# Kernel optimization log

Measured on AMD Instinct MI355X. Metric: run time of the kernel, lower is better.

Reference implementation:

```python
import jax, jax.numpy as jnp
import numpy as np

NEG_SLOPE = 0.01  # F.leaky_relu default


def grid_sample_bilinear(im, pts):
    """torch.nn.functional.grid_sample equivalent, mode='bilinear',
    align_corners=True, padding_mode='zeros'.
    im: [B, C, H, W], pts: [B, N, 2] in [-1, 1] (x, y order). Returns [B, C, N].
    """
    B, C, H, W = im.shape
    x = (pts[..., 0] + 1.0) * 0.5 * (W - 1)  # [B, N]
    y = (pts[..., 1] + 1.0) * 0.5 * (H - 1)
    x0 = jnp.floor(x)
    y0 = jnp.floor(y)
    wx1 = x - x0
    wy1 = y - y0
    wx0 = 1.0 - wx1
    wy0 = 1.0 - wy1
    x0i = x0.astype(jnp.int32)
    y0i = y0.astype(jnp.int32)
    x1i = x0i + 1
    y1i = y0i + 1

    def corner(yi, xi, w):
        valid = (xi >= 0) & (xi < W) & (yi >= 0) & (yi < H)
        yc = jnp.clip(yi, 0, H - 1)
        xc = jnp.clip(xi, 0, W - 1)
        # gather per-batch: [B, C, N]
        g = jax.vmap(lambda f, yy, xx: f[:, yy, xx])(im, yc, xc)
        return g * (w * valid.astype(im.dtype))[:, None, :]

    return (corner(y0i, x0i, wy0 * wx0) + corner(y0i, x1i, wy0 * wx1)
            + corner(y1i, x0i, wy1 * wx0) + corner(y1i, x1i, wy1 * wx1))


def conv1x1(x, w, b):
    # x: [B, Cin, N], w: [Cout, Cin], b: [Cout] -> [B, Cout, N]
    return jnp.einsum('oi,bin->bon', w, x) + b[None, :, None]


def setup_inputs() -> dict:
    key = jax.random.key(0)
    ks = jax.random.split(key, 9)
    B, N, C, H, W = 64, 6890, 256, 56, 56
    filter_channels = [256, 128, 64, 5]
    points = jax.random.uniform(ks[0], (B, N, 2), jnp.float32, -1.0, 1.0)
    im_feat = jax.random.normal(ks[1], (B, C, H, W), jnp.float32)

    def mk_conv(k, cin, cout):
        k1, k2 = jax.random.split(k)
        bound = 1.0 / np.sqrt(cin)
        w = jax.random.uniform(k1, (cout, cin), jnp.float32, -bound, bound)
        b = jax.random.uniform(k2, (cout,), jnp.float32, -bound, bound)
        return w, b

    w0, b0 = mk_conv(ks[2], filter_channels[0], filter_channels[1])
    w1, b1 = mk_conv(ks[3], filter_channels[1] + filter_channels[0], filter_channels[2])
    w2, b2 = mk_conv(ks[4], filter_channels[2] + filter_channels[0], filter_channels[3])
    return {"points": points, "im_feat": im_feat,
            "w0": w0, "b0": b0, "w1": w1, "b1": b1, "w2": w2, "b2": b2}


def reference(points, im_feat, w0, b0, w1, b1, w2, b2):
    # sampling: bilinear gather of point-wise features, [B, C_s, N]
    point_feat = grid_sample_bilinear(im_feat, points)
    # reduce_dim: 1x1 conv MLP with skip-concat of the input features
    y = jax.nn.leaky_relu(conv1x1(point_feat, w0, b0), NEG_SLOPE)
    y = jax.nn.leaky_relu(conv1x1(jnp.concatenate([y, point_feat], axis=1), w1, b1), NEG_SLOPE)
    y = conv1x1(jnp.concatenate([y, point_feat], axis=1), w2, b2)  # last layer: no leaky_relu
    y = jax.nn.relu(y)  # self.last_op
    mesh_align_feat = y.reshape(y.shape[0], -1)  # [B, C_p * N]
    return (mesh_align_feat, point_feat)
```

## Files before the change

kernel.cpp:

```cpp
#include <hip/hip_runtime.h>

#define B_    64
#define C_    256
#define H_    56
#define W_    56
#define N_    6890
#define HW_   3136
#define NTILE 108

#define WB1_OFF (128*256)
#define WB2_OFF (128*256 + 64*384)
#define WTOT    (128*256 + 64*384 + 5*320)

typedef __attribute__((ext_vector_type(8))) __bf16 bf16x8;
typedef __attribute__((ext_vector_type(8))) unsigned short ushort8;
typedef __attribute__((ext_vector_type(4))) float f32x4;
typedef __attribute__((ext_vector_type(2))) float f32x2;
typedef __attribute__((ext_vector_type(4))) unsigned int uint4v;
typedef __attribute__((ext_vector_type(2))) unsigned int uint2v;

__device__ __forceinline__ unsigned short f2bf(float f) {
    unsigned int u = __builtin_bit_cast(unsigned int, f);
    u += 0x7FFFu + ((u >> 16) & 1u);
    return (unsigned short)(u >> 16);
}
__device__ __forceinline__ unsigned int pack2(float lo, float hi) {
    return (unsigned int)f2bf(lo) | ((unsigned int)f2bf(hi) << 16);
}
__device__ __forceinline__ float leaky(float v) { return v > 0.f ? v : 0.01f * v; }
__device__ __forceinline__ int pswz(int p) { return p ^ ((p >> 3) & 7); }

__global__ void wconv_kernel(const float* __restrict__ w0, const float* __restrict__ w1,
                             const float* __restrict__ w2, unsigned short* __restrict__ wb) {
    int i = blockIdx.x * 256 + threadIdx.x;
    if (i >= WTOT) return;
    float v = (i < WB1_OFF) ? w0[i] : (i < WB2_OFF) ? w1[i - WB1_OFF] : w2[i - WB2_OFF];
    wb[i] = f2bf(v);
}

__global__ __launch_bounds__(256) void transpose_kernel(
    const float* __restrict__ im, float* __restrict__ imT) {
    __shared__ float Lt[64][68];
    const int t   = threadIdx.x;
    const int bid = blockIdx.x;
    const int xcd  = bid & 7;
    const int rest = bid >> 3;
    const int b    = ((rest & 7) << 3) + xcd;
    const int tl   = rest >> 3;
    const int pt   = tl % 49, ct = tl / 49;
    const int p0   = pt * 64, c0 = ct * 64;

    const float* src = im + ((size_t)b * C_ + c0) * HW_ + p0;
#pragma unroll
    for (int rr = 0; rr < 4; rr++) {
        int c_loc = (t >> 4) + rr * 16;
        int pq    = (t & 15) << 2;
        f32x4 v = *(const f32x4*)(src + (size_t)c_loc * HW_ + pq);
        Lt[c_loc][pq]     = v[0];
        Lt[c_loc][pq + 1] = v[1];
        Lt[c_loc][pq + 2] = v[2];
        Lt[c_loc][pq + 3] = v[3];
    }
    __syncthreads();
    float* dst = imT + ((size_t)b * HW_ + p0) * C_ + c0;
#pragma unroll
    for (int i = 0; i < 4; i++) {
        int idx = t + (i << 8);
        int pr  = idx >> 4;
        int c4  = (idx & 15) << 2;
        f32x4 v;
        v[0] = Lt[c4][pr]; v[1] = Lt[c4 + 1][pr];
        v[2] = Lt[c4 + 2][pr]; v[3] = Lt[c4 + 3][pr];
        *(f32x4*)(dst + (size_t)pr * C_ + c4) = v;
    }
}

__device__ __forceinline__ bf16x8 bfrag(const unsigned int* buf, int rowstride_dw,
                                        int n, int k0) {
    int cd = (k0 >> 1) ^ ((n & 7) << 2);
    uint4v v = *(const uint4v*)(buf + n * rowstride_dw + cd);
    return __builtin_bit_cast(bf16x8, v);
}
__device__ __forceinline__ bf16x8 afrag_bf(const unsigned short* __restrict__ wb, int ldk,
                                           int rowbase, int k0, int lane, int nrows) {
    int i = rowbase + (lane & 15);
    int k = k0 + ((lane >> 4) << 3);
    if (i < nrows) return __builtin_bit_cast(bf16x8, *(const ushort8*)(wb + (size_t)i * ldk + k));
    ushort8 z = {0, 0, 0, 0, 0, 0, 0, 0};
    return __builtin_bit_cast(bf16x8, z);
}

__global__ __launch_bounds__(256, 2) void fused_kernel(
    const float* __restrict__ points, const float* __restrict__ imT,
    const float* __restrict__ b0_, const float* __restrict__ b1,
    const float* __restrict__ b2, const unsigned short* __restrict__ wb,
    float* __restrict__ out0, float* __restrict__ out1) {
    __shared__ float Ls[16384];
    __shared__ float Pw[64][4];
    __shared__ int   Pi[64][2];

    const int t    = threadIdx.x;
    const int lane = t & 63;
    const int wave = t >> 6;
    const int bid  = blockIdx.x;
    const int xcd  = bid & 7;
    const int rr   = bid >> 3;
    const int tile = rr % NTILE;
    const int b    = (rr / NTILE) * 8 + xcd;
    const int n0   = tile * 64;

    if (t < 64) {
        int n = min(n0 + t, N_ - 1);
        f32x2 pt = *(const f32x2*)(points + ((size_t)b * N_ + n) * 2);
        float fx = fminf(fmaxf((pt.x + 1.f) * 27.5f, 0.f), 55.f);
        float fy = fminf(fmaxf((pt.y + 1.f) * 27.5f, 0.f), 55.f);
        float x0f = floorf(fx), y0f = floorf(fy);
        int x0 = (int)x0f, y0 = (int)y0f;
        float wx1 = fx - x0f, wy1 = fy - y0f;
        float wx0 = 1.f - wx1, wy0 = 1.f - wy1;
        bool hix = x0 >= W_ - 1;
        int   xb  = hix ? W_ - 2 : x0;
        float wxl = hix ? 0.f : wx0;
        float wxr = hix ? wx0 : wx1;
        int y0c = min(y0, H_ - 1);
        int y1c = min(y0 + 1, H_ - 1);
        Pw[t][0] = wy0 * wxl; Pw[t][1] = wy0 * wxr;
        Pw[t][2] = wy1 * wxl; Pw[t][3] = wy1 * wxr;
        Pi[t][0] = y0c * W_ + xb; Pi[t][1] = y1c * W_ + xb;
    }
    __syncthreads();

    const float* ib = imT + (size_t)b * HW_ * C_;
#pragma unroll
    for (int i = 0; i < 16; i += 2) {
        int pA = wave * 16 + i, pB = pA + 1;
        float wA0 = Pw[pA][0], wA1 = Pw[pA][1], wA2 = Pw[pA][2], wA3 = Pw[pA][3];
        float wB0 = Pw[pB][0], wB1 = Pw[pB][1], wB2 = Pw[pB][2], wB3 = Pw[pB][3];
        int aA0 = Pi[pA][0], aA1 = Pi[pA][1];
        int aB0 = Pi[pB][0], aB1 = Pi[pB][1];
        const float* sA0 = ib + ((size_t)aA0 << 8) + (lane << 2);
        const float* sA1 = ib + ((size_t)aA1 << 8) + (lane << 2);
        const float* sB0 = ib + ((size_t)aB0 << 8) + (lane << 2);
        const float* sB1 = ib + ((size_t)aB1 << 8) + (lane << 2);
        f32x4 cA00 = *(const f32x4*)(sA0);
        f32x4 cA01 = *(const f32x4*)(sA0 + 256);
        f32x4 cA10 = *(const f32x4*)(sA1);
        f32x4 cA11 = *(const f32x4*)(sA1 + 256);
        f32x4 cB00 = *(const f32x4*)(sB0);
        f32x4 cB01 = *(const f32x4*)(sB0 + 256);
        f32x4 cB10 = *(const f32x4*)(sB1);
        f32x4 cB11 = *(const f32x4*)(sB1 + 256);
        f32x4 vA, vB;
#pragma unroll
        for (int j = 0; j < 4; j++) {
            vA[j] = wA0 * cA00[j] + wA1 * cA01[j] + wA2 * cA10[j] + wA3 * cA11[j];
            vB[j] = wB0 * cB00[j] + wB1 * cB01[j] + wB2 * cB10[j] + wB3 * cB11[j];
        }
        *(f32x4*)(Ls + pA * 256 + ((lane ^ (pA & 7)) << 2)) = vA;
        *(f32x4*)(Ls + pB * 256 + ((lane ^ (pB & 7)) << 2)) = vB;
    }
    __syncthreads();

    f32x4 xr[16];
#pragma unroll
    for (int q = 0; q < 16; q++) {
        int qd = (wave * 16 + q) ^ (lane & 7);
        xr[q] = *(const f32x4*)(Ls + lane * 256 + (qd << 2));
    }
    __syncthreads();

    unsigned int* Xs  = (unsigned int*)Ls;
    unsigned int* Y0s = (unsigned int*)Ls + 8192;
    {
        float* pfb = out1 + (size_t)b * C_ * N_ + n0;
        const bool okn = (n0 + lane) < N_;
        const int swz = (lane & 7) << 2;
#pragma unroll
        for (int q = 0; q < 16; q += 2) {
            int c0 = wave * 64 + q * 4;
            if (okn) {
#pragma unroll
                for (int jj = 0; jj < 4; jj++) {
                    pfb[(size_t)(c0 + jj) * N_ + lane]     = xr[q][jj];
                    pfb[(size_t)(c0 + 4 + jj) * N_ + lane] = xr[q + 1][jj];
                }
            }
            uint4v pk;
            pk[0] = pack2(xr[q][0], xr[q][1]);     pk[1] = pack2(xr[q][2], xr[q][3]);
            pk[2] = pack2(xr[q + 1][0], xr[q + 1][1]); pk[3] = pack2(xr[q + 1][2], xr[q + 1][3]);
            *(uint4v*)(Xs + lane * 128 + ((c0 >> 1) ^ swz)) = pk;
        }
    }

    bf16x8 a1[2][8];
#pragma unroll
    for (int mt = 0; mt < 2; mt++)
#pragma unroll
        for (int ks = 0; ks < 8; ks++)
            a1[mt][ks] = afrag_bf(wb, 256, (wave * 2 + mt) * 16, ks * 32, lane, 1 << 30);

    __syncthreads();

    const int cl = lane & 15;
    const int rh = lane >> 4;
    const int kq = rh << 3;

    f32x4 acc1[2][4] = {};
#pragma unroll
    for (int ks = 0; ks < 8; ks++) {
        bf16x8 bx[4];
#pragma unroll
        for (int nt = 0; nt < 4; nt++)
            bx[nt] = bfrag(Xs, 128, nt * 16 + cl, ks * 32 + kq);
#pragma unroll
        for (int mt = 0; mt < 2; mt++)
#pragma unroll
            for (int nt = 0; nt < 4; nt++)
                acc1[mt][nt] = __builtin_amdgcn_mfma_f32_16x16x32_bf16(
                    a1[mt][ks], bx[nt], acc1[mt][nt], 0, 0, 0);
    }

#pragma unroll
    for (int mt = 0; mt < 2; mt++) {
        int m0 = (wave * 2 + mt) * 16 + (rh << 2);
        f32x4 bias = *(const f32x4*)(b0_ + m0);
#pragma unroll
        for (int nt = 0; nt < 4; nt++) {
            int nn = nt * 16 + cl;
            float v0 = leaky(acc1[mt][nt][0] + bias[0]);
            float v1 = leaky(acc1[mt][nt][1] + bias[1]);
            float v2 = leaky(acc1[mt][nt][2] + bias[2]);
            float v3 = leaky(acc1[mt][nt][3] + bias[3]);
            int md = (m0 >> 1) ^ ((nn & 7) << 2);
            uint2v pk; pk[0] = pack2(v0, v1); pk[1] = pack2(v2, v3);
            *(uint2v*)(Y0s + nn * 64 + md) = pk;
        }
    }

    bf16x8 a2[12];
#pragma unroll
    for (int ks = 0; ks < 12; ks++)
        a2[ks] = afrag_bf(wb + WB1_OFF, 384, wave * 16, ks * 32, lane, 1 << 30);

    __syncthreads();

    f32x4 acc2[4] = {};
#pragma unroll
    for (int ks = 0; ks < 12; ks++) {
#pragma unroll
        for (int nt = 0; nt < 4; nt++) {
            bf16x8 bx = (ks < 4) ? bfrag(Y0s, 64, nt * 16 + cl, ks * 32 + kq)
                                 : bfrag(Xs, 128, nt * 16 + cl, (ks - 4) * 32 + kq);
            acc2[nt] = __builtin_amdgcn_mfma_f32_16x16x32_bf16(a2[ks], bx, acc2[nt], 0, 0, 0);
        }
    }

    bf16x8 a3[10];
#pragma unroll
    for (int ks = 0; ks < 10; ks++)
        a3[ks] = afrag_bf(wb + WB2_OFF, 320, 0, ks * 32, lane, 5);

    __syncthreads();

    {
        int m0 = wave * 16 + (rh << 2);
        f32x4 bias = *(const f32x4*)(b1 + m0);
#pragma unroll
        for (int nt = 0; nt < 4; nt++) {
            int nn = nt * 16 + cl;
            float v0 = leaky(acc2[nt][0] + bias[0]);
            float v1 = leaky(acc2[nt][1] + bias[1]);
            float v2 = leaky(acc2[nt][2] + bias[2]);
            float v3 = leaky(acc2[nt][3] + bias[3]);
            int md = (m0 >> 1) ^ ((nn & 7) << 2);
            uint2v pk; pk[0] = pack2(v0, v1); pk[1] = pack2(v2, v3);
            *(uint2v*)(Y0s + nn * 32 + md) = pk;
        }
    }

    __syncthreads();

    {
        int nn = wave * 16 + cl;
        f32x4 acc3 = {};
#pragma unroll
        for (int ks = 0; ks < 10; ks++) {
            bf16x8 bx = (ks < 2) ? bfrag(Y0s, 32, nn, ks * 32 + kq)
                                 : bfrag(Xs, 128, nn, (ks - 2) * 32 + kq);
            acc3 = __builtin_amdgcn_mfma_f32_16x16x32_bf16(a3[ks], bx, acc3, 0, 0, 0);
        }
        int gn2 = n0 + nn;
        if (gn2 < N_) {
#pragma unroll
            for (int r2 = 0; r2 < 4; r2++) {
                int m = (rh << 2) + r2;
                if (m < 5) {
                    float v = acc3[r2] + b2[m];
                    v = v > 0.f ? v : 0.f;
                    out0[((size_t)b * 5 + m) * N_ + gn2] = v;
                }
            }
        }
    }
}

__global__ __launch_bounds__(512, 6) void gather_kernel(
    const float* __restrict__ points, const float* __restrict__ im,
    float* __restrict__ out1) {
    __shared__ float Lg[HW_ * 4];
    const int t   = threadIdx.x;
    const int bid = blockIdx.x;
    const int b  = ((bid & 7) << 3) | ((bid >> 3) & 7);
    const int ch = bid >> 6;
    const f32x4* im4 = (const f32x4*)(im + ((size_t)b * C_ + ch * 4) * HW_);
#pragma unroll
    for (int g0 = 0; g0 < 2; g0++) {
        int g = t + (g0 << 9);
        if (g < 784) {
            f32x4 r0 = im4[g], r1 = im4[784 + g], r2 = im4[1568 + g], r3 = im4[2352 + g];
#pragma unroll
            for (int i = 0; i < 4; i++) {
                f32x4 v; v[0] = r0[i]; v[1] = r1[i]; v[2] = r2[i]; v[3] = r3[i];
                *(f32x4*)(Lg + (pswz((g << 2) + i) << 2)) = v;
            }
        }
    }
    __syncthreads();
    const float* ptb = points + (size_t)b * N_ * 2;
    const size_t ob0 = ((size_t)b * C_ + ch * 4) * N_;
#pragma unroll 2
    for (int p = 0; p < 14; p++) {
        int n = t + (p << 9);
        if (n < N_) {
            f32x2 pt = *(const f32x2*)(ptb + 2 * n);
            float fx = fminf(fmaxf((pt.x + 1.f) * 27.5f, 0.f), 55.f);
            float fy = fminf(fmaxf((pt.y + 1.f) * 27.5f, 0.f), 55.f);
            float x0f = floorf(fx), y0f = floorf(fy);
            int x0 = (int)x0f, y0 = (int)y0f;
            float wx1 = fx - x0f, wy1 = fy - y0f;
            float wx0 = 1.f - wx1, wy0 = 1.f - wy1;
            bool hix = x0 >= W_ - 1;
            int   xb  = hix ? W_ - 2 : x0;
            float wxl = hix ? 0.f : wx0;
            float wxr = hix ? wx0 : wx1;
            int y0c = min(y0, H_ - 1);
            int y1c = min(y0 + 1, H_ - 1);
            float w00 = wy0 * wxl, w01 = wy0 * wxr, w10 = wy1 * wxl, w11 = wy1 * wxr;
            int ia0 = y0c * W_ + xb, ia1 = y1c * W_ + xb;
            f32x4 q00 = *(const f32x4*)(Lg + (pswz(ia0)     << 2));
            f32x4 q01 = *(const f32x4*)(Lg + (pswz(ia0 + 1) << 2));
            f32x4 q10 = *(const f32x4*)(Lg + (pswz(ia1)     << 2));
            f32x4 q11 = *(const f32x4*)(Lg + (pswz(ia1 + 1) << 2));
            out1[ob0 + n]        = w00*q00[0] + w01*q01[0] + w10*q10[0] + w11*q11[0];
            out1[ob0 + N_ + n]   = w00*q00[1] + w01*q01[1] + w10*q10[1] + w11*q11[1];
            out1[ob0 + 2*N_ + n] = w00*q00[2] + w01*q01[2] + w10*q10[2] + w11*q11[2];
            out1[ob0 + 3*N_ + n] = w00*q00[3] + w01*q01[3] + w10*q10[3] + w11*q11[3];
        }
    }
}

__device__ __forceinline__ bf16x8 afrag_f32(const float* __restrict__ wp, int ldk,
                                            int rowbase, int k0, int lane, int nrows) {
    int i = rowbase + (lane & 15);
    int k = k0 + ((lane >> 4) << 3);
    ushort8 u;
    if (i < nrows) {
        const float* s = wp + (size_t)i * ldk + k;
#pragma unroll
        for (int j = 0; j < 8; j++) u[j] = f2bf(s[j]);
    } else {
#pragma unroll
        for (int j = 0; j < 8; j++) u[j] = 0;
    }
    return __builtin_bit_cast(bf16x8, u);
}

template <bool BF16W>
__global__ __launch_bounds__(256) void mlp_kernel(
    const float* __restrict__ pf,
    const float* __restrict__ w0, const float* __restrict__ b0_,
    const float* __restrict__ w1, const float* __restrict__ b1,
    const float* __restrict__ w2, const float* __restrict__ b2,
    const unsigned short* __restrict__ wb,
    float* __restrict__ out0) {
    __shared__ unsigned int Xs[64 * 128];
    __shared__ unsigned int Y0s[64 * 64];
    const int t    = threadIdx.x;
    const int lane = t & 63;
    const int wave = t >> 6;
    const int bid  = blockIdx.x;
    const int b    = bid / NTILE;
    const int tile = bid - b * NTILE;
    const int n0   = tile * 64;
    const int nn_g = min(n0 + lane, N_ - 1);
    const int swz  = (lane & 7) << 2;
    const float* pfb = pf + (size_t)b * C_ * N_;
#pragma unroll
    for (int g8 = 0; g8 < 8; g8++) {
        int c0 = wave * 64 + g8 * 8;
        float v[8];
#pragma unroll
        for (int j = 0; j < 8; j++) v[j] = pfb[(size_t)(c0 + j) * N_ + nn_g];
        uint4v pk;
        pk[0] = pack2(v[0], v[1]); pk[1] = pack2(v[2], v[3]);
        pk[2] = pack2(v[4], v[5]); pk[3] = pack2(v[6], v[7]);
        *(uint4v*)(Xs + lane * 128 + ((c0 >> 1) ^ swz)) = pk;
    }
    bf16x8 a1[2][8];
#pragma unroll
    for (int mt = 0; mt < 2; mt++)
#pragma unroll
        for (int ks = 0; ks < 8; ks++)
            a1[mt][ks] = BF16W ? afrag_bf(wb, 256, (wave * 2 + mt) * 16, ks * 32, lane, 1 << 30)
                               : afrag_f32(w0, 256, (wave * 2 + mt) * 16, ks * 32, lane, 1 << 30);
    __syncthreads();
    const int cl = lane & 15;
    const int rh = lane >> 4;
    const int kq = rh << 3;
    f32x4 acc1[2][4] = {};
#pragma unroll
    for (int ks = 0; ks < 8; ks++) {
        bf16x8 bx[4];
#pragma unroll
        for (int nt = 0; nt < 4; nt++)
            bx[nt] = bfrag(Xs, 128, nt * 16 + cl, ks * 32 + kq);
#pragma unroll
        for (int mt = 0; mt < 2; mt++)
#pragma unroll
            for (int nt = 0; nt < 4; nt++)
                acc1[mt][nt] = __builtin_amdgcn_mfma_f32_16x16x32_bf16(
                    a1[mt][ks], bx[nt], acc1[mt][nt], 0, 0, 0);
    }
#pragma unroll
    for (int mt = 0; mt < 2; mt++) {
        int m0 = (wave * 2 + mt) * 16 + (rh << 2);
        f32x4 bias = *(const f32x4*)(b0_ + m0);
#pragma unroll
        for (int nt = 0; nt < 4; nt++) {
            int nn = nt * 16 + cl;
            float v0 = leaky(acc1[mt][nt][0] + bias[0]);
            float v1 = leaky(acc1[mt][nt][1] + bias[1]);
            float v2 = leaky(acc1[mt][nt][2] + bias[2]);
            float v3 = leaky(acc1[mt][nt][3] + bias[3]);
            int md = (m0 >> 1) ^ ((nn & 7) << 2);
            uint2v pk; pk[0] = pack2(v0, v1); pk[1] = pack2(v2, v3);
            *(uint2v*)(Y0s + nn * 64 + md) = pk;
        }
    }
    bf16x8 a2[12];
#pragma unroll
    for (int ks = 0; ks < 12; ks++)
        a2[ks] = BF16W ? afrag_bf(wb + WB1_OFF, 384, wave * 16, ks * 32, lane, 1 << 30)
                       : afrag_f32(w1, 384, wave * 16, ks * 32, lane, 1 << 30);
    __syncthreads();
    f32x4 acc2[4] = {};
#pragma unroll
    for (int ks = 0; ks < 12; ks++) {
#pragma unroll
        for (int nt = 0; nt < 4; nt++) {
            bf16x8 bx = (ks < 4) ? bfrag(Y0s, 64, nt * 16 + cl, ks * 32 + kq)
                                 : bfrag(Xs, 128, nt * 16 + cl, (ks - 4) * 32 + kq);
            acc2[nt] = __builtin_amdgcn_mfma_f32_16x16x32_bf16(a2[ks], bx, acc2[nt], 0, 0, 0);
        }
    }
    bf16x8 a3[10];
#pragma unroll
    for (int ks = 0; ks < 10; ks++)
        a3[ks] = BF16W ? afrag_bf(wb + WB2_OFF, 320, 0, ks * 32, lane, 5)
                       : afrag_f32(w2, 320, 0, ks * 32, lane, 5);
    __syncthreads();
    {
        int m0 = wave * 16 + (rh << 2);
        f32x4 bias = *(const f32x4*)(b1 + m0);
#pragma unroll
        for (int nt = 0; nt < 4; nt++) {
            int nn = nt * 16 + cl;
            float v0 = leaky(acc2[nt][0] + bias[0]);
            float v1 = leaky(acc2[nt][1] + bias[1]);
            float v2 = leaky(acc2[nt][2] + bias[2]);
            float v3 = leaky(acc2[nt][3] + bias[3]);
            int md = (m0 >> 1) ^ ((nn & 7) << 2);
            uint2v pk; pk[0] = pack2(v0, v1); pk[1] = pack2(v2, v3);
            *(uint2v*)(Y0s + nn * 32 + md) = pk;
        }
    }
    __syncthreads();
    {
        int nn = wave * 16 + cl;
        f32x4 acc3 = {};
#pragma unroll
        for (int ks = 0; ks < 10; ks++) {
            bf16x8 bx = (ks < 2) ? bfrag(Y0s, 32, nn, ks * 32 + kq)
                                 : bfrag(Xs, 128, nn, (ks - 2) * 32 + kq);
            acc3 = __builtin_amdgcn_mfma_f32_16x16x32_bf16(a3[ks], bx, acc3, 0, 0, 0);
        }
        int gn2 = n0 + nn;
        if (gn2 < N_) {
#pragma unroll
            for (int r2 = 0; r2 < 4; r2++) {
                int m = (rh << 2) + r2;
                if (m < 5) {
                    float v = acc3[r2] + b2[m];
                    v = v > 0.f ? v : 0.f;
                    out0[((size_t)b * 5 + m) * N_ + gn2] = v;
                }
            }
        }
    }
}

extern "C" void kernel_launch(void* const* d_in, const int* in_sizes, int n_in,
                              void* d_out, int out_size, void* d_ws, size_t ws_size,
                              hipStream_t stream) {
    const float* points = (const float*)d_in[0];
    const float* im     = (const float*)d_in[1];
    const float* w0     = (const float*)d_in[2];
    const float* b0     = (const float*)d_in[3];
    const float* w1     = (const float*)d_in[4];
    const float* b1     = (const float*)d_in[5];
    const float* w2     = (const float*)d_in[6];
    const float* b2     = (const float*)d_in[7];
    float* out0 = (float*)d_out;
    float* out1 = out0 + (size_t)B_ * 5 * N_;

    const size_t TBYTES = (size_t)B_ * HW_ * C_ * 4;
    const size_t WBYTES = (size_t)WTOT * 2;
    const bool fok = (d_ws != nullptr) && (ws_size >= TBYTES + WBYTES);
    const bool wok = fok || ((d_ws != nullptr) && (ws_size >= WBYTES));
    float*          imT = (float*)d_ws;
    unsigned short* wb  = fok ? (unsigned short*)((char*)d_ws + TBYTES)
                              : (unsigned short*)d_ws;

    if (wok) {
        hipLaunchKernelGGL(wconv_kernel, dim3((WTOT + 255) / 256), dim3(256), 0, stream,
                           w0, w1, w2, wb);
    }
    if (fok) {
        hipLaunchKernelGGL(transpose_kernel, dim3(B_ * 196), dim3(256), 0, stream, im, imT);
        hipLaunchKernelGGL(fused_kernel, dim3(B_ * NTILE), dim3(256), 0, stream,
                           points, imT, b0, b1, b2, wb, out0, out1);
    } else {
        hipLaunchKernelGGL(gather_kernel, dim3(B_ * 64), dim3(512), 0, stream,
                           points, im, out1);
        if (wok) {
            hipLaunchKernelGGL(mlp_kernel<true>, dim3(B_ * NTILE), dim3(256), 0, stream,
                               out1, w0, b0, w1, b1, w2, b2, wb, out0);
        } else {
            hipLaunchKernelGGL(mlp_kernel<false>, dim3(B_ * NTILE), dim3(256), 0, stream,
                               out1, w0, b0, w1, b1, w2, b2,
                               (const unsigned short*)nullptr, out0);
        }
    }
}
```

Before: 393.0 us.

## Replace image transpose with LDS-staged channel-slice gather into bf16 intermediate

The channel-last fp32 image transpose and the global-memory corner gathers inside the fused kernel are removed. A new gather kernel stages a 4-channel slice of one batch image in LDS, samples every point from LDS, and writes a packed bf16 intermediate. The MLP kernel then reads that intermediate, expands it to fp32 for the point_feat output, and feeds the MFMA layers. This replaces the large transpose round trip and scattered global reads with coalesced streaming. The cost is an extra intermediate write and read, and point_feat values are now rounded to bf16, which reduces output precision.

```diff
diff --git a/kernel.cpp b/kernel.cpp
--- a/kernel.cpp
+++ b/kernel.cpp
@@ -27,6 +27,12 @@
 __device__ __forceinline__ unsigned int pack2(float lo, float hi) {
     return (unsigned int)f2bf(lo) | ((unsigned int)f2bf(hi) << 16);
 }
+__device__ __forceinline__ float bflo(unsigned int u) {
+    return __builtin_bit_cast(float, u << 16);
+}
+__device__ __forceinline__ float bfhi(unsigned int u) {
+    return __builtin_bit_cast(float, u & 0xffff0000u);
+}
 __device__ __forceinline__ float leaky(float v) { return v > 0.f ? v : 0.01f * v; }
 __device__ __forceinline__ int pswz(int p) { return p ^ ((p >> 3) & 7); }
 
@@ -38,49 +44,68 @@
     wb[i] = f2bf(v);
 }
 
-__global__ __launch_bounds__(256) void transpose_kernel(
-    const float* __restrict__ im, float* __restrict__ imT) {
-    __shared__ float Lt[64][68];
+__global__ __launch_bounds__(512, 6) void gather_c(
+    const float* __restrict__ points, const float* __restrict__ im,
+    unsigned int* __restrict__ x2) {
+    __shared__ float Ls[HW_ * 4];
+
     const int t   = threadIdx.x;
     const int bid = blockIdx.x;
-    const int xcd  = bid & 7;
-    const int rest = bid >> 3;
-    const int b    = ((rest & 7) << 3) + xcd;
-    const int tl   = rest >> 3;
-    const int pt   = tl % 49, ct = tl / 49;
-    const int p0   = pt * 64, c0 = ct * 64;
-
-    const float* src = im + ((size_t)b * C_ + c0) * HW_ + p0;
-#pragma unroll
-    for (int rr = 0; rr < 4; rr++) {
-        int c_loc = (t >> 4) + rr * 16;
-        int pq    = (t & 15) << 2;
-        f32x4 v = *(const f32x4*)(src + (size_t)c_loc * HW_ + pq);
-        Lt[c_loc][pq]     = v[0];
-        Lt[c_loc][pq + 1] = v[1];
-        Lt[c_loc][pq + 2] = v[2];
-        Lt[c_loc][pq + 3] = v[3];
-    }
-    __syncthreads();
-    float* dst = imT + ((size_t)b * HW_ + p0) * C_ + c0;
-#pragma unroll
-    for (int i = 0; i < 4; i++) {
-        int idx = t + (i << 8);
-        int pr  = idx >> 4;
-        int c4  = (idx & 15) << 2;
-        f32x4 v;
-        v[0] = Lt[c4][pr]; v[1] = Lt[c4 + 1][pr];
-        v[2] = Lt[c4 + 2][pr]; v[3] = Lt[c4 + 3][pr];
-        *(f32x4*)(dst + (size_t)pr * C_ + c4) = v;
-    }
-}
-
-__device__ __forceinline__ bf16x8 bfrag(const unsigned int* buf, int rowstride_dw,
-                                        int n, int k0) {
-    int cd = (k0 >> 1) ^ ((n & 7) << 2);
-    uint4v v = *(const uint4v*)(buf + n * rowstride_dw + cd);
-    return __builtin_bit_cast(bf16x8, v);
-}
+    const int b  = ((bid & 7) << 3) | ((bid >> 3) & 7);
+    const int ch = bid >> 6;
+
+    const f32x4* im4 = (const f32x4*)(im + ((size_t)b * C_ + ch * 4) * HW_);
+#pragma unroll
+    for (int g0 = 0; g0 < 2; g0++) {
+        int g = t + (g0 << 9);
+        if (g < 784) {
+            f32x4 r0 = im4[g], r1 = im4[784 + g], r2 = im4[1568 + g], r3 = im4[2352 + g];
+#pragma unroll
+            for (int i = 0; i < 4; i++) {
+                f32x4 v; v[0] = r0[i]; v[1] = r1[i]; v[2] = r2[i]; v[3] = r3[i];
+                *(f32x4*)(Ls + (pswz((g << 2) + i) << 2)) = v;
+            }
+        }
+    }
+    __syncthreads();
+
+    const float* ptb = points + (size_t)b * N_ * 2;
+    unsigned int* xout = x2 + ((size_t)((b << 6) + ch) * N_) * 2;
+#pragma unroll 2
+    for (int p = 0; p < 14; p++) {
+        int n = t + (p << 9);
+        if (n < N_) {
+            f32x2 pt = *(const f32x2*)(ptb + 2 * n);
+            float fx = fminf(fmaxf((pt.x + 1.f) * 27.5f, 0.f), 55.f);
+            float fy = fminf(fmaxf((pt.y + 1.f) * 27.5f, 0.f), 55.f);
+            float x0f = floorf(fx), y0f = floorf(fy);
+            int x0 = (int)x0f, y0 = (int)y0f;
+            float wx1 = fx - x0f, wy1 = fy - y0f;
+            float wx0 = 1.f - wx1, wy0 = 1.f - wy1;
+            bool hix = x0 >= W_ - 1;
+            int   xb  = hix ? W_ - 2 : x0;
+            float wxl = hix ? 0.f : wx0;
+            float wxr = hix ? wx0 : wx1;
+            int y0c = min(y0, H_ - 1);
+            int y1c = min(y0 + 1, H_ - 1);
+            float w00 = wy0 * wxl, w01 = wy0 * wxr;
+            float w10 = wy1 * wxl, w11 = wy1 * wxr;
+            int ia0 = y0c * W_ + xb, ia1 = y1c * W_ + xb;
+
+            f32x4 q00 = *(const f32x4*)(Ls + (pswz(ia0)     << 2));
+            f32x4 q01 = *(const f32x4*)(Ls + (pswz(ia0 + 1) << 2));
+            f32x4 q10 = *(const f32x4*)(Ls + (pswz(ia1)     << 2));
+            f32x4 q11 = *(const f32x4*)(Ls + (pswz(ia1 + 1) << 2));
+            float v0 = w00*q00[0] + w01*q01[0] + w10*q10[0] + w11*q11[0];
+            float v1 = w00*q00[1] + w01*q01[1] + w10*q10[1] + w11*q11[1];
+            float v2 = w00*q00[2] + w01*q01[2] + w10*q10[2] + w11*q11[2];
+            float v3 = w00*q00[3] + w01*q01[3] + w10*q10[3] + w11*q11[3];
+            uint2v pk; pk[0] = pack2(v0, v1); pk[1] = pack2(v2, v3);
+            *(uint2v*)(xout + (size_t)n * 2) = pk;
+        }
+    }
+}
+
 __device__ __forceinline__ bf16x8 afrag_bf(const unsigned short* __restrict__ wb, int ldk,
                                            int rowbase, int k0, int lane, int nrows) {
     int i = rowbase + (lane & 15);
@@ -89,107 +114,53 @@
     ushort8 z = {0, 0, 0, 0, 0, 0, 0, 0};
     return __builtin_bit_cast(bf16x8, z);
 }
-
-__global__ __launch_bounds__(256, 2) void fused_kernel(
-    const float* __restrict__ points, const float* __restrict__ imT,
+__device__ __forceinline__ bf16x8 bfrag(const unsigned int* buf, int rowstride_dw,
+                                        int n, int k0) {
+    int cd = (k0 >> 1) ^ ((n & 7) << 2);
+    uint4v v = *(const uint4v*)(buf + n * rowstride_dw + cd);
+    return __builtin_bit_cast(bf16x8, v);
+}
+
+__global__ __launch_bounds__(256) void mlp_c(
+    const unsigned int* __restrict__ x2,
     const float* __restrict__ b0_, const float* __restrict__ b1,
     const float* __restrict__ b2, const unsigned short* __restrict__ wb,
     float* __restrict__ out0, float* __restrict__ out1) {
-    __shared__ float Ls[16384];
-    __shared__ float Pw[64][4];
-    __shared__ int   Pi[64][2];
+    __shared__ unsigned int Xs[64 * 128];
+    __shared__ unsigned int Y0s[64 * 64];
 
     const int t    = threadIdx.x;
     const int lane = t & 63;
     const int wave = t >> 6;
     const int bid  = blockIdx.x;
-    const int xcd  = bid & 7;
-    const int rr   = bid >> 3;
-    const int tile = rr % NTILE;
-    const int b    = (rr / NTILE) * 8 + xcd;
+    const int b    = bid / NTILE;
+    const int tile = bid - b * NTILE;
     const int n0   = tile * 64;
 
-    if (t < 64) {
-        int n = min(n0 + t, N_ - 1);
-        f32x2 pt = *(const f32x2*)(points + ((size_t)b * N_ + n) * 2);
-        float fx = fminf(fmaxf((pt.x + 1.f) * 27.5f, 0.f), 55.f);
-        float fy = fminf(fmaxf((pt.y + 1.f) * 27.5f, 0.f), 55.f);
-        float x0f = floorf(fx), y0f = floorf(fy);
-        int x0 = (int)x0f, y0 = (int)y0f;
-        float wx1 = fx - x0f, wy1 = fy - y0f;
-        float wx0 = 1.f - wx1, wy0 = 1.f - wy1;
-        bool hix = x0 >= W_ - 1;
-        int   xb  = hix ? W_ - 2 : x0;
-        float wxl = hix ? 0.f : wx0;
-        float wxr = hix ? wx0 : wx1;
-        int y0c = min(y0, H_ - 1);
-        int y1c = min(y0 + 1, H_ - 1);
-        Pw[t][0] = wy0 * wxl; Pw[t][1] = wy0 * wxr;
-        Pw[t][2] = wy1 * wxl; Pw[t][3] = wy1 * wxr;
-        Pi[t][0] = y0c * W_ + xb; Pi[t][1] = y1c * W_ + xb;
-    }
-    __syncthreads();
-
-    const float* ib = imT + (size_t)b * HW_ * C_;
-#pragma unroll
-    for (int i = 0; i < 16; i += 2) {
-        int pA = wave * 16 + i, pB = pA + 1;
-        float wA0 = Pw[pA][0], wA1 = Pw[pA][1], wA2 = Pw[pA][2], wA3 = Pw[pA][3];
-        float wB0 = Pw[pB][0], wB1 = Pw[pB][1], wB2 = Pw[pB][2], wB3 = Pw[pB][3];
-        int aA0 = Pi[pA][0], aA1 = Pi[pA][1];
-        int aB0 = Pi[pB][0], aB1 = Pi[pB][1];
-        const float* sA0 = ib + ((size_t)aA0 << 8) + (lane << 2);
-        const float* sA1 = ib + ((size_t)aA1 << 8) + (lane << 2);
-        const float* sB0 = ib + ((size_t)aB0 << 8) + (lane << 2);
-        const float* sB1 = ib + ((size_t)aB1 << 8) + (lane << 2);
-        f32x4 cA00 = *(const f32x4*)(sA0);
-        f32x4 cA01 = *(const f32x4*)(sA0 + 256);
-        f32x4 cA10 = *(const f32x4*)(sA1);
-        f32x4 cA11 = *(const f32x4*)(sA1 + 256);
-        f32x4 cB00 = *(const f32x4*)(sB0);
-        f32x4 cB01 = *(const f32x4*)(sB0 + 256);
-        f32x4 cB10 = *(const f32x4*)(sB1);
-        f32x4 cB11 = *(const f32x4*)(sB1 + 256);
-        f32x4 vA, vB;
-#pragma unroll
-        for (int j = 0; j < 4; j++) {
-            vA[j] = wA0 * cA00[j] + wA1 * cA01[j] + wA2 * cA10[j] + wA3 * cA11[j];
-            vB[j] = wB0 * cB00[j] + wB1 * cB01[j] + wB2 * cB10[j] + wB3 * cB11[j];
-        }
-        *(f32x4*)(Ls + pA * 256 + ((lane ^ (pA & 7)) << 2)) = vA;
-        *(f32x4*)(Ls + pB * 256 + ((lane ^ (pB & 7)) << 2)) = vB;
-    }
-    __syncthreads();
-
-    f32x4 xr[16];
-#pragma unroll
-    for (int q = 0; q < 16; q++) {
-        int qd = (wave * 16 + q) ^ (lane & 7);
-        xr[q] = *(const f32x4*)(Ls + lane * 256 + (qd << 2));
-    }
-    __syncthreads();
-
-    unsigned int* Xs  = (unsigned int*)Ls;
-    unsigned int* Y0s = (unsigned int*)Ls + 8192;
-    {
-        float* pfb = out1 + (size_t)b * C_ * N_ + n0;
-        const bool okn = (n0 + lane) < N_;
-        const int swz = (lane & 7) << 2;
-#pragma unroll
-        for (int q = 0; q < 16; q += 2) {
-            int c0 = wave * 64 + q * 4;
-            if (okn) {
-#pragma unroll
-                for (int jj = 0; jj < 4; jj++) {
-                    pfb[(size_t)(c0 + jj) * N_ + lane]     = xr[q][jj];
-                    pfb[(size_t)(c0 + 4 + jj) * N_ + lane] = xr[q + 1][jj];
-                }
-            }
-            uint4v pk;
-            pk[0] = pack2(xr[q][0], xr[q][1]);     pk[1] = pack2(xr[q][2], xr[q][3]);
-            pk[2] = pack2(xr[q + 1][0], xr[q + 1][1]); pk[3] = pack2(xr[q + 1][2], xr[q + 1][3]);
-            *(uint4v*)(Xs + lane * 128 + ((c0 >> 1) ^ swz)) = pk;
-        }
+    const int  nn_g = min(n0 + lane, N_ - 1);
+    const bool okn  = (n0 + lane) < N_;
+    const int  swz  = (lane & 7) << 2;
+
+    float* pfb = out1 + (size_t)b * C_ * N_ + n0;
+#pragma unroll
+    for (int j = 0; j < 8; j++) {
+        int d2a = wave * 16 + 2 * j;
+        const unsigned int* src = x2 + ((size_t)((b << 6) + d2a) * N_ + nn_g) * 2;
+        uint2v q0 = *(const uint2v*)src;
+        uint2v q1 = *(const uint2v*)(src + 2 * (size_t)N_);
+        if (okn) {
+            int c0 = 4 * d2a;
+            pfb[(size_t)(c0    ) * N_ + lane] = bflo(q0[0]);
+            pfb[(size_t)(c0 + 1) * N_ + lane] = bfhi(q0[0]);
+            pfb[(size_t)(c0 + 2) * N_ + lane] = bflo(q0[1]);
+            pfb[(size_t)(c0 + 3) * N_ + lane] = bfhi(q0[1]);
+            pfb[(size_t)(c0 + 4) * N_ + lane] = bflo(q1[0]);
+            pfb[(size_t)(c0 + 5) * N_ + lane] = bfhi(q1[0]);
+            pfb[(size_t)(c0 + 6) * N_ + lane] = bflo(q1[1]);
+            pfb[(size_t)(c0 + 7) * N_ + lane] = bfhi(q1[1]);
+        }
+        uint4v pk; pk[0] = q0[0]; pk[1] = q0[1]; pk[2] = q1[0]; pk[3] = q1[1];
+        *(uint4v*)(Xs + lane * 128 + ((wave * 32 + 4 * j) ^ swz)) = pk;
     }
 
     bf16x8 a1[2][8];
@@ -375,13 +346,11 @@
     return __builtin_bit_cast(bf16x8, u);
 }
 
-template <bool BF16W>
-__global__ __launch_bounds__(256) void mlp_kernel(
+__global__ __launch_bounds__(256) void mlp_fallback(
     const float* __restrict__ pf,
     const float* __restrict__ w0, const float* __restrict__ b0_,
     const float* __restrict__ w1, const float* __restrict__ b1,
     const float* __restrict__ w2, const float* __restrict__ b2,
-    const unsigned short* __restrict__ wb,
     float* __restrict__ out0) {
     __shared__ unsigned int Xs[64 * 128];
     __shared__ unsigned int Y0s[64 * 64];
@@ -411,8 +380,7 @@
     for (int mt = 0; mt < 2; mt++)
 #pragma unroll
         for (int ks = 0; ks < 8; ks++)
-            a1[mt][ks] = BF16W ? afrag_bf(wb, 256, (wave * 2 + mt) * 16, ks * 32, lane, 1 << 30)
-                               : afrag_f32(w0, 256, (wave * 2 + mt) * 16, ks * 32, lane, 1 << 30);
+            a1[mt][ks] = afrag_f32(w0, 256, (wave * 2 + mt) * 16, ks * 32, lane, 1 << 30);
     __syncthreads();
     const int cl = lane & 15;
     const int rh = lane >> 4;
@@ -450,8 +418,7 @@
     bf16x8 a2[12];
 #pragma unroll
     for (int ks = 0; ks < 12; ks++)
-        a2[ks] = BF16W ? afrag_bf(wb + WB1_OFF, 384, wave * 16, ks * 32, lane, 1 << 30)
-                       : afrag_f32(w1, 384, wave * 16, ks * 32, lane, 1 << 30);
+        a2[ks] = afrag_f32(w1, 384, wave * 16, ks * 32, lane, 1 << 30);
     __syncthreads();
     f32x4 acc2[4] = {};
 #pragma unroll
@@ -466,8 +433,7 @@
     bf16x8 a3[10];
 #pragma unroll
     for (int ks = 0; ks < 10; ks++)
-        a3[ks] = BF16W ? afrag_bf(wb + WB2_OFF, 320, 0, ks * 32, lane, 5)
-                       : afrag_f32(w2, 320, 0, ks * 32, lane, 5);
+        a3[ks] = afrag_f32(w2, 320, 0, ks * 32, lane, 5);
     __syncthreads();
     {
         int m0 = wave * 16 + (rh << 2);
@@ -523,32 +489,23 @@
     float* out0 = (float*)d_out;
     float* out1 = out0 + (size_t)B_ * 5 * N_;
 
-    const size_t TBYTES = (size_t)B_ * HW_ * C_ * 4;
+    const size_t XBYTES = (size_t)B_ * 64 * N_ * 8;
     const size_t WBYTES = (size_t)WTOT * 2;
-    const bool fok = (d_ws != nullptr) && (ws_size >= TBYTES + WBYTES);
-    const bool wok = fok || ((d_ws != nullptr) && (ws_size >= WBYTES));
-    float*          imT = (float*)d_ws;
-    unsigned short* wb  = fok ? (unsigned short*)((char*)d_ws + TBYTES)
-                              : (unsigned short*)d_ws;
-
-    if (wok) {
+    const bool cok = (d_ws != nullptr) && (ws_size >= XBYTES + WBYTES);
+    unsigned int*   x2 = (unsigned int*)d_ws;
+    unsigned short* wb = (unsigned short*)((char*)d_ws + XBYTES);
+
+    if (cok) {
         hipLaunchKernelGGL(wconv_kernel, dim3((WTOT + 255) / 256), dim3(256), 0, stream,
                            w0, w1, w2, wb);
-    }
-    if (fok) {
-        hipLaunchKernelGGL(transpose_kernel, dim3(B_ * 196), dim3(256), 0, stream, im, imT);
-        hipLaunchKernelGGL(fused_kernel, dim3(B_ * NTILE), dim3(256), 0, stream,
-                           points, imT, b0, b1, b2, wb, out0, out1);
+        hipLaunchKernelGGL(gather_c, dim3(B_ * 64), dim3(512), 0, stream,
+                           points, im, x2);
+        hipLaunchKernelGGL(mlp_c, dim3(B_ * NTILE), dim3(256), 0, stream,
+                           x2, b0, b1, b2, wb, out0, out1);
     } else {
         hipLaunchKernelGGL(gather_kernel, dim3(B_ * 64), dim3(512), 0, stream,
                            points, im, out1);
-        if (wok) {
-            hipLaunchKernelGGL(mlp_kernel<true>, dim3(B_ * NTILE), dim3(256), 0, stream,
-                               out1, w0, b0, w1, b1, w2, b2, wb, out0);
-        } else {
-            hipLaunchKernelGGL(mlp_kernel<false>, dim3(B_ * NTILE), dim3(256), 0, stream,
-                               out1, w0, b0, w1, b1, w2, b2,
-                               (const unsigned short*)nullptr, out0);
-        }
-    }
-}
+        hipLaunchKernelGGL(mlp_fallback, dim3(B_ * NTILE), dim3(256), 0, stream,
+                           out1, w0, b0, w1, b1, w2, b2, out0);
+    }
+}
```

Result: faster. 382.5 us (-2.7%).
